# Performance work log

Hardware: AMD Instinct MI355X
Metric: run time of the kernel (lower is better)

## Reference

```python
import jax, jax.numpy as jnp
import numpy as np

GAMMA = 2.5
K = 4
RHO = 0.085
TAU_CLIP = 5.0
NUM_HEADS = 8


def setup_inputs() -> dict:
    key = jax.random.key(0)
    ks = jax.random.split(key, 4)
    B, T, C = 2, 2048, 512
    x = jax.random.normal(ks[0], (B, T, C), jnp.float32)
    tau = jax.random.uniform(ks[1], (B, T, T), jnp.float32)
    s = 1.0 / np.sqrt(C)
    Wqkv = jax.random.normal(ks[2], (C, 3 * C), jnp.float32) * s
    bqkv = jnp.zeros((3 * C,), jnp.float32)
    Wproj = jax.random.normal(ks[3], (C, C), jnp.float32) * s
    bproj = jnp.zeros((C,), jnp.float32)
    return dict(x=x, tau=tau, Wqkv=Wqkv, bqkv=bqkv, Wproj=Wproj, bproj=bproj)


def reference(x, tau, Wqkv, bqkv, Wproj, bproj):
    B, T, C = x.shape
    H = NUM_HEADS
    D = C // H
    qkv = x @ Wqkv + bqkv                       # [B,T,3C]
    q, k, v = jnp.split(qkv, 3, axis=-1)
    q = q.reshape(B, T, H, D).transpose(0, 2, 1, 3)   # [B,H,T,D]
    k = k.reshape(B, T, H, D).transpose(0, 2, 1, 3)
    v = v.reshape(B, T, H, D).transpose(0, 2, 1, 3)
    scale = D ** -0.5
    logits = jnp.einsum('bhtd,bhsd->bhts', q, k) * scale   # [B,H,T,T]
    pheromone_bias = GAMMA * jnp.log(tau + 1e-8)           # [B,T,T]
    logits = logits + pheromone_bias[:, None]
    # top-K keys per query from tau define the sparse mask (LOCAL_WINDOW=0)
    k_val = min(K, T)
    idx = jax.lax.top_k(tau, k_val)[1]                     # [B,T,K]
    mask = jnp.zeros((B, T, T), bool).at[
        jnp.arange(B)[:, None, None], jnp.arange(T)[None, :, None], idx
    ].set(True)
    logits = jnp.where(mask[:, None], logits, -jnp.inf)
    attn = jax.nn.softmax(logits, axis=-1)                 # [B,H,T,T]
    # EMA pheromone (tau) update, no gradient in original (torch.no_grad)
    signal = attn.mean(axis=1)                             # [B,T,T]
    tau_new = (1.0 - RHO) * tau + signal ** 3
    tau_new = tau_new / (tau_new.sum(axis=-1, keepdims=True) + 1e-8)
    tau_new = jnp.minimum(tau_new, TAU_CLIP)
    tau_new = jax.lax.stop_gradient(tau_new)
    out = jnp.einsum('bhts,bhsd->bthd', attn, v).reshape(B, T, C)
    out = out @ Wproj + bproj
    return out, tau_new
```

## Files before the change

kernel.cpp:

```cpp
#include <hip/hip_runtime.h>
#include <hip/hip_bf16.h>
#include <math.h>

#define BB 2
#define TT 2048
#define CC 512
#define HH 8
#define DD 64
#define KK 4
#define C3 1536
#define MROWS (BB*TT)

#define G1_NT (C3/64)
#define G1_BLOCKS (G1_NT*(MROWS/128))
#define G2_NT (CC/64)
#define G2_BLOCKS (G2_NT*(MROWS/128))

typedef __attribute__((ext_vector_type(8))) short bf16x8;
typedef __attribute__((ext_vector_type(4))) float floatx4;

static __device__ __forceinline__ unsigned short f2bf(float f) {
  unsigned int u = __float_as_uint(f);
  return (unsigned short)((u + 0x7fffu + ((u >> 16) & 1u)) >> 16);
}
static __device__ __forceinline__ float bf2f(unsigned short u) {
  return __uint_as_float(((unsigned int)u) << 16);
}

template<bool BF16OUT>
static __device__ __forceinline__ void gemm_body(
    int bid, int nt,
    const unsigned short* __restrict__ A,
    const unsigned short* __restrict__ Bt,
    const float* __restrict__ bias,
    void* __restrict__ Cout, int N, int K) {
  __shared__ bf16x8 As[128 * 4];
  __shared__ bf16x8 Bs[64 * 4];
  const int tid  = threadIdx.x;
  const int wave = tid >> 6;
  const int lane = tid & 63;
  const int n0 = (bid % nt) * 64;
  const int m0 = (bid / nt) * 128;
  const int m_off = (wave >> 1) * 64;
  const int n_off = (wave & 1) * 32;
  const int lrow = lane >> 2;
  const int lcol = (lane & 3) * 8;
  const int fr = lane & 15;
  const int fq = lane >> 4;

  floatx4 acc[4][2];
#pragma unroll
  for (int i = 0; i < 4; ++i)
#pragma unroll
    for (int j = 0; j < 2; ++j) acc[i][j] = (floatx4){0.f, 0.f, 0.f, 0.f};

  for (int k0 = 0; k0 < K; k0 += 32) {
#pragma unroll
    for (int s = 0; s < 2; ++s) {
      int q = wave * 2 + s;
      const unsigned short* ga = A + (size_t)(m0 + q * 16 + lrow) * K + k0 + lcol;
      __builtin_amdgcn_global_load_lds(
          (const __attribute__((address_space(1))) void*)ga,
          (__attribute__((address_space(3))) void*)((char*)As + q * 1024), 16, 0, 0);
    }
    const unsigned short* gb = Bt + (size_t)(n0 + wave * 16 + lrow) * K + k0 + lcol;
    __builtin_amdgcn_global_load_lds(
        (const __attribute__((address_space(1))) void*)gb,
        (__attribute__((address_space(3))) void*)((char*)Bs + wave * 1024), 16, 0, 0);
    __syncthreads();
    bf16x8 a[4], b[2];
#pragma unroll
    for (int i = 0; i < 4; ++i) a[i] = As[(m_off + i * 16 + fr) * 4 + fq];
#pragma unroll
    for (int j = 0; j < 2; ++j) b[j] = Bs[(n_off + j * 16 + fr) * 4 + fq];
#pragma unroll
    for (int i = 0; i < 4; ++i)
#pragma unroll
      for (int j = 0; j < 2; ++j)
        acc[i][j] = __builtin_amdgcn_mfma_f32_16x16x32_bf16(a[i], b[j], acc[i][j], 0, 0, 0);
    __syncthreads();
  }
#pragma unroll
  for (int j = 0; j < 2; ++j) {
    int col = n0 + n_off + j * 16 + fr;
    float bv = bias[col];
#pragma unroll
    for (int i = 0; i < 4; ++i) {
#pragma unroll
      for (int r = 0; r < 4; ++r) {
        int row = m0 + m_off + i * 16 + fq * 4 + r;
        float v = acc[i][j][r] + bv;
        if (BF16OUT) ((unsigned short*)Cout)[(size_t)row * N + col] = f2bf(v);
        else         ((float*)Cout)[(size_t)row * N + col] = v;
      }
    }
  }
}

static __device__ __forceinline__ void topk_body(
    int row, const float* __restrict__ tau, int* __restrict__ idx_out) {
  const int tid = threadIdx.x;
  const float4* rp = (const float4*)(tau + (size_t)row * TT);
  float v[8];
  float4 f0 = rp[tid * 2], f1 = rp[tid * 2 + 1];
  v[0]=f0.x; v[1]=f0.y; v[2]=f0.z; v[3]=f0.w;
  v[4]=f1.x; v[5]=f1.y; v[6]=f1.z; v[7]=f1.w;
  __shared__ float wv[4];
  __shared__ int wi[4];
  __shared__ int winner;
  const int base = tid * 8;
  int chosen[KK];
  for (int r = 0; r < KK; ++r) {
    float bv = v[0]; int bi = base;
#pragma unroll
    for (int i = 1; i < 8; ++i)
      if (v[i] > bv) { bv = v[i]; bi = base + i; }
#pragma unroll
    for (int off = 32; off > 0; off >>= 1) {
      float vv = __shfl_xor(bv, off, 64);
      int   ii = __shfl_xor(bi, off, 64);
      if (vv > bv || (vv == bv && ii < bi)) { bv = vv; bi = ii; }
    }
    if ((tid & 63) == 0) { wv[tid >> 6] = bv; wi[tid >> 6] = bi; }
    __syncthreads();
    if (tid == 0) {
      float b2 = wv[0]; int i2 = wi[0];
      for (int k = 1; k < 4; ++k)
        if (wv[k] > b2 || (wv[k] == b2 && wi[k] < i2)) { b2 = wv[k]; i2 = wi[k]; }
      winner = i2;
    }
    __syncthreads();
    int win = winner;
    chosen[r] = win;
    if ((win >> 3) == tid) v[win & 7] = -1e30f;
    __syncthreads();
  }
  if (tid < KK) idx_out[row * KK + tid] = chosen[tid];
}

static __device__ __forceinline__ void tau_body(
    int row, const float* __restrict__ tau, const int* __restrict__ idx_in,
    const float* __restrict__ sig_in, float* __restrict__ tau_out) {
  const int tid = threadIdx.x;
  int i4[KK]; float s3[KK];
#pragma unroll
  for (int j = 0; j < KK; ++j) {
    i4[j] = idx_in[row * KK + j];
    float s = sig_in[row * KK + j];
    s3[j] = s * s * s;
  }
  const float4* rp = (const float4*)(tau + (size_t)row * TT);
  float v[8];
  float4 f0 = rp[tid * 2], f1 = rp[tid * 2 + 1];
  v[0]=f0.x; v[1]=f0.y; v[2]=f0.z; v[3]=f0.w;
  v[4]=f1.x; v[5]=f1.y; v[6]=f1.z; v[7]=f1.w;
  const float keep = 1.0f - 0.085f;
  const int base = tid * 8;
  float local = 0.f;
#pragma unroll
  for (int i = 0; i < 8; ++i) {
    float t = keep * v[i];
#pragma unroll
    for (int j = 0; j < KK; ++j)
      if (base + i == i4[j]) t += s3[j];
    v[i] = t;
    local += t;
  }
#pragma unroll
  for (int off = 32; off > 0; off >>= 1) local += __shfl_xor(local, off, 64);
  __shared__ float wsum[4];
  __shared__ float tot;
  if ((tid & 63) == 0) wsum[tid >> 6] = local;
  __syncthreads();
  if (tid == 0) tot = wsum[0] + wsum[1] + wsum[2] + wsum[3];
  __syncthreads();
  float inv = 1.f / (tot + 1e-8f);
  float4* op = (float4*)(tau_out + (size_t)row * TT);
  float4 o0 = { fminf(v[0]*inv,5.f), fminf(v[1]*inv,5.f), fminf(v[2]*inv,5.f), fminf(v[3]*inv,5.f) };
  float4 o1 = { fminf(v[4]*inv,5.f), fminf(v[5]*inv,5.f), fminf(v[6]*inv,5.f), fminf(v[7]*inv,5.f) };
  op[tid * 2] = o0;
  op[tid * 2 + 1] = o1;
}

static __device__ __forceinline__ void transpose_body(
    int t, int nbx, const float* __restrict__ W, unsigned short* __restrict__ Wt,
    int R, int Cn) {
  __shared__ unsigned short tile[32][33];
  const int c0 = (t % nbx) * 32, r0 = (t / nbx) * 32;
  const int tx = threadIdx.x & 31, ty = threadIdx.x >> 5;
#pragma unroll
  for (int i = 0; i < 4; ++i) {
    int r = ty + i * 8;
    tile[r][tx] = f2bf(W[(size_t)(r0 + r) * Cn + c0 + tx]);
  }
  __syncthreads();
#pragma unroll
  for (int i = 0; i < 4; ++i) {
    int r = ty + i * 8;
    Wt[(size_t)(c0 + r) * R + r0 + tx] = tile[tx][r];
  }
}

__global__ __launch_bounds__(256) void prep_kernel(
    const float* __restrict__ x, unsigned short* __restrict__ x_bf,
    const float* __restrict__ Wqkv, unsigned short* __restrict__ wqkv_t,
    const float* __restrict__ Wproj, unsigned short* __restrict__ wproj_t) {
  const int bid = blockIdx.x;
  if (bid < 1024) {
    int g = bid * 256 + threadIdx.x;
    const float4* p = (const float4*)x;
    float4 f0 = p[g * 2], f1 = p[g * 2 + 1];
    union { unsigned short u[8]; uint4 v; } pk;
    pk.u[0]=f2bf(f0.x); pk.u[1]=f2bf(f0.y); pk.u[2]=f2bf(f0.z); pk.u[3]=f2bf(f0.w);
    pk.u[4]=f2bf(f1.x); pk.u[5]=f2bf(f1.y); pk.u[6]=f2bf(f1.z); pk.u[7]=f2bf(f1.w);
    ((uint4*)x_bf)[g] = pk.v;
  } else if (bid < 1024 + 768) {
    transpose_body(bid - 1024, C3 / 32, Wqkv, wqkv_t, CC, C3);
  } else {
    transpose_body(bid - 1792, CC / 32, Wproj, wproj_t, CC, CC);
  }
}

__global__ __launch_bounds__(256) void gemm1_topk_kernel(
    const unsigned short* __restrict__ x_bf,
    const unsigned short* __restrict__ wqkv_t,
    const float* __restrict__ bqkv, unsigned short* __restrict__ qkv_bf,
    const float* __restrict__ tau, int* __restrict__ idx_out) {
  if (blockIdx.x < G1_BLOCKS)
    gemm_body<true>(blockIdx.x, G1_NT, x_bf, wqkv_t, bqkv, qkv_bf, C3, CC);
  else
    topk_body(blockIdx.x - G1_BLOCKS, tau, idx_out);
}

__global__ __launch_bounds__(512) void attn_kernel(
    const unsigned short* __restrict__ qkv, const float* __restrict__ tau,
    const int* __restrict__ idx_in, unsigned short* __restrict__ attn_bf,
    float* __restrict__ sig_out) {
  const int row  = blockIdx.x;
  const int b    = row >> 11;
  const int tid  = threadIdx.x;
  const int h    = tid >> 6;
  const int lane = tid & 63;

  __shared__ int   idx4[KK];
  __shared__ float tau4[KK];
  __shared__ float ps[HH][KK];
  if (tid < KK) {
    int s = idx_in[row * KK + tid];
    idx4[tid] = s;
    tau4[tid] = tau[(size_t)row * TT + s];
  }
  __syncthreads();

  const float q = bf2f(qkv[(size_t)row * C3 + h * DD + lane]);
  int   sidx[KK];
  float logit[KK];
#pragma unroll
  for (int j = 0; j < KK; ++j) {
    sidx[j] = idx4[j];
    float kv = bf2f(qkv[((size_t)(b * TT + sidx[j])) * C3 + CC + h * DD + lane]);
    float p = q * kv;
#pragma unroll
    for (int off = 32; off > 0; off >>= 1) p += __shfl_xor(p, off, 64);
    logit[j] = p * 0.125f + 2.5f * logf(tau4[j] + 1e-8f);
  }

  float m = fmaxf(fmaxf(logit[0], logit[1]), fmaxf(logit[2], logit[3]));
  float p[KK], den = 0.f;
#pragma unroll
  for (int j = 0; j < KK; ++j) { p[j] = expf(logit[j] - m); den += p[j]; }
  float inv = 1.f / den;
#pragma unroll
  for (int j = 0; j < KK; ++j) p[j] *= inv;

  float o = 0.f;
#pragma unroll
  for (int j = 0; j < KK; ++j)
    o += p[j] * bf2f(qkv[((size_t)(b * TT + sidx[j])) * C3 + 2 * CC + h * DD + lane]);
  attn_bf[(size_t)row * CC + h * DD + lane] = f2bf(o);

  if (lane < KK) ps[h][lane] = p[lane];
  __syncthreads();
  if (tid < KK) {
    float s = 0.f;
#pragma unroll
    for (int k = 0; k < HH; ++k) s += ps[k][tid];
    sig_out[row * KK + tid] = s * (1.0f / HH);
  }
}

__global__ __launch_bounds__(256) void gemm2_tau_kernel(
    const unsigned short* __restrict__ attn_bf,
    const unsigned short* __restrict__ wproj_t,
    const float* __restrict__ bproj, float* __restrict__ out,
    const float* __restrict__ tau, const int* __restrict__ idx_in,
    const float* __restrict__ sig_in, float* __restrict__ tau_out) {
  if (blockIdx.x < G2_BLOCKS)
    gemm_body<false>(blockIdx.x, G2_NT, attn_bf, wproj_t, bproj, out, CC, CC);
  else
    tau_body(blockIdx.x - G2_BLOCKS, tau, idx_in, sig_in, tau_out);
}

extern "C" void kernel_launch(void* const* d_in, const int* in_sizes, int n_in,
                              void* d_out, int out_size, void* d_ws, size_t ws_size,
                              hipStream_t stream) {
  const float* x     = (const float*)d_in[0];
  const float* tau   = (const float*)d_in[1];
  const float* Wqkv  = (const float*)d_in[2];
  const float* bqkv  = (const float*)d_in[3];
  const float* Wproj = (const float*)d_in[4];
  const float* bproj = (const float*)d_in[5];

  float* out     = (float*)d_out;
  float* tau_new = out + (size_t)MROWS * CC;

  char* w = (char*)d_ws;
  unsigned short* qkv_bf  = (unsigned short*)w; w += (size_t)MROWS * C3 * 2;
  unsigned short* x_bf    = (unsigned short*)w; w += (size_t)MROWS * CC * 2;
  unsigned short* wqkv_t  = (unsigned short*)w; w += (size_t)C3 * CC * 2;
  unsigned short* wproj_t = (unsigned short*)w; w += (size_t)CC * CC * 2;
  unsigned short* attn_bf = (unsigned short*)w; w += (size_t)MROWS * CC * 2;
  int*   idx = (int*)w;                  w += (size_t)MROWS * KK * 4;
  float* sig = (float*)w;

  prep_kernel<<<2048, 256, 0, stream>>>(x, x_bf, Wqkv, wqkv_t, Wproj, wproj_t);

  gemm1_topk_kernel<<<G1_BLOCKS + MROWS, 256, 0, stream>>>(
      x_bf, wqkv_t, bqkv, qkv_bf, tau, idx);

  attn_kernel<<<MROWS, 512, 0, stream>>>(qkv_bf, tau, idx, attn_bf, sig);

  gemm2_tau_kernel<<<G2_BLOCKS + MROWS, 256, 0, stream>>>(
      attn_bf, wproj_t, bproj, out, tau, idx, sig, tau_new);
}
```

Baseline: 150.6 us.

## Widen GEMM tiles to 128x128, use nontemporal stores, batch attention gathers

The GEMM tiles grow from 128x64 to 128x128 per block, so each wave computes a 64x64 sub-tile with 16 MFMAs per k-step, which doubles A-tile reuse and halves the block count. Float outputs and the tau_out rows are written with nontemporal stores to avoid polluting the cache. In the sparse attention kernel, all K and V gathers are issued up front and the four dot-product reductions are interleaved, which exposes memory and shuffle parallelism. The cost is fewer blocks (less occupancy and tail balance) and more accumulator registers.

```diff
diff --git a/kernel.cpp b/kernel.cpp
--- a/kernel.cpp
+++ b/kernel.cpp
@@ -11,9 +11,9 @@
 #define C3 1536
 #define MROWS (BB*TT)
 
-#define G1_NT (C3/64)
+#define G1_NT (C3/128)
 #define G1_BLOCKS (G1_NT*(MROWS/128))
-#define G2_NT (CC/64)
+#define G2_NT (CC/128)
 #define G2_BLOCKS (G2_NT*(MROWS/128))
 
 typedef __attribute__((ext_vector_type(8))) short bf16x8;
@@ -35,24 +35,24 @@
     const float* __restrict__ bias,
     void* __restrict__ Cout, int N, int K) {
   __shared__ bf16x8 As[128 * 4];
-  __shared__ bf16x8 Bs[64 * 4];
+  __shared__ bf16x8 Bs[128 * 4];
   const int tid  = threadIdx.x;
   const int wave = tid >> 6;
   const int lane = tid & 63;
-  const int n0 = (bid % nt) * 64;
+  const int n0 = (bid % nt) * 128;
   const int m0 = (bid / nt) * 128;
   const int m_off = (wave >> 1) * 64;
-  const int n_off = (wave & 1) * 32;
+  const int n_off = (wave & 1) * 64;
   const int lrow = lane >> 2;
   const int lcol = (lane & 3) * 8;
   const int fr = lane & 15;
   const int fq = lane >> 4;
 
-  floatx4 acc[4][2];
+  floatx4 acc[4][4];
 #pragma unroll
   for (int i = 0; i < 4; ++i)
 #pragma unroll
-    for (int j = 0; j < 2; ++j) acc[i][j] = (floatx4){0.f, 0.f, 0.f, 0.f};
+    for (int j = 0; j < 4; ++j) acc[i][j] = (floatx4){0.f, 0.f, 0.f, 0.f};
 
   for (int k0 = 0; k0 < K; k0 += 32) {
 #pragma unroll
@@ -62,26 +62,26 @@
       __builtin_amdgcn_global_load_lds(
           (const __attribute__((address_space(1))) void*)ga,
           (__attribute__((address_space(3))) void*)((char*)As + q * 1024), 16, 0, 0);
+      const unsigned short* gb = Bt + (size_t)(n0 + q * 16 + lrow) * K + k0 + lcol;
+      __builtin_amdgcn_global_load_lds(
+          (const __attribute__((address_space(1))) void*)gb,
+          (__attribute__((address_space(3))) void*)((char*)Bs + q * 1024), 16, 0, 0);
     }
-    const unsigned short* gb = Bt + (size_t)(n0 + wave * 16 + lrow) * K + k0 + lcol;
-    __builtin_amdgcn_global_load_lds(
-        (const __attribute__((address_space(1))) void*)gb,
-        (__attribute__((address_space(3))) void*)((char*)Bs + wave * 1024), 16, 0, 0);
-    __syncthreads();
-    bf16x8 a[4], b[2];
+    __syncthreads();
+    bf16x8 a[4], b[4];
 #pragma unroll
     for (int i = 0; i < 4; ++i) a[i] = As[(m_off + i * 16 + fr) * 4 + fq];
 #pragma unroll
-    for (int j = 0; j < 2; ++j) b[j] = Bs[(n_off + j * 16 + fr) * 4 + fq];
+    for (int j = 0; j < 4; ++j) b[j] = Bs[(n_off + j * 16 + fr) * 4 + fq];
 #pragma unroll
     for (int i = 0; i < 4; ++i)
 #pragma unroll
-      for (int j = 0; j < 2; ++j)
+      for (int j = 0; j < 4; ++j)
         acc[i][j] = __builtin_amdgcn_mfma_f32_16x16x32_bf16(a[i], b[j], acc[i][j], 0, 0, 0);
     __syncthreads();
   }
 #pragma unroll
-  for (int j = 0; j < 2; ++j) {
+  for (int j = 0; j < 4; ++j) {
     int col = n0 + n_off + j * 16 + fr;
     float bv = bias[col];
 #pragma unroll
@@ -91,7 +91,10 @@
         int row = m0 + m_off + i * 16 + fq * 4 + r;
         float v = acc[i][j][r] + bv;
         if (BF16OUT) ((unsigned short*)Cout)[(size_t)row * N + col] = f2bf(v);
-        else         ((float*)Cout)[(size_t)row * N + col] = v;
+        else {
+          float* p = (float*)Cout + (size_t)row * N + col;
+          __builtin_nontemporal_store(v, p);
+        }
       }
     }
   }
@@ -175,11 +178,11 @@
   if (tid == 0) tot = wsum[0] + wsum[1] + wsum[2] + wsum[3];
   __syncthreads();
   float inv = 1.f / (tot + 1e-8f);
-  float4* op = (float4*)(tau_out + (size_t)row * TT);
-  float4 o0 = { fminf(v[0]*inv,5.f), fminf(v[1]*inv,5.f), fminf(v[2]*inv,5.f), fminf(v[3]*inv,5.f) };
-  float4 o1 = { fminf(v[4]*inv,5.f), fminf(v[5]*inv,5.f), fminf(v[6]*inv,5.f), fminf(v[7]*inv,5.f) };
-  op[tid * 2] = o0;
-  op[tid * 2 + 1] = o1;
+  floatx4* op = (floatx4*)(tau_out + (size_t)row * TT);
+  floatx4 o0 = { fminf(v[0]*inv,5.f), fminf(v[1]*inv,5.f), fminf(v[2]*inv,5.f), fminf(v[3]*inv,5.f) };
+  floatx4 o1 = { fminf(v[4]*inv,5.f), fminf(v[5]*inv,5.f), fminf(v[6]*inv,5.f), fminf(v[7]*inv,5.f) };
+  __builtin_nontemporal_store(o0, op + tid * 2);
+  __builtin_nontemporal_store(o1, op + tid * 2 + 1);
 }
 
 static __device__ __forceinline__ void transpose_body(
@@ -253,20 +256,29 @@
   __syncthreads();
 
   const float q = bf2f(qkv[(size_t)row * C3 + h * DD + lane]);
-  int   sidx[KK];
+  float kv[KK], vv[KK];
+#pragma unroll
+  for (int j = 0; j < KK; ++j) {
+    size_t bs = ((size_t)(b * TT + idx4[j])) * C3 + h * DD + lane;
+    kv[j] = bf2f(qkv[bs + CC]);
+    vv[j] = bf2f(qkv[bs + 2 * CC]);
+  }
+
+  float p[KK];
+#pragma unroll
+  for (int j = 0; j < KK; ++j) p[j] = q * kv[j];
+#pragma unroll
+  for (int off = 32; off > 0; off >>= 1)
+#pragma unroll
+    for (int j = 0; j < KK; ++j) p[j] += __shfl_xor(p[j], off, 64);
+
   float logit[KK];
 #pragma unroll
-  for (int j = 0; j < KK; ++j) {
-    sidx[j] = idx4[j];
-    float kv = bf2f(qkv[((size_t)(b * TT + sidx[j])) * C3 + CC + h * DD + lane]);
-    float p = q * kv;
-#pragma unroll
-    for (int off = 32; off > 0; off >>= 1) p += __shfl_xor(p, off, 64);
-    logit[j] = p * 0.125f + 2.5f * logf(tau4[j] + 1e-8f);
-  }
+  for (int j = 0; j < KK; ++j)
+    logit[j] = p[j] * 0.125f + 2.5f * logf(tau4[j] + 1e-8f);
 
   float m = fmaxf(fmaxf(logit[0], logit[1]), fmaxf(logit[2], logit[3]));
-  float p[KK], den = 0.f;
+  float den = 0.f;
 #pragma unroll
   for (int j = 0; j < KK; ++j) { p[j] = expf(logit[j] - m); den += p[j]; }
   float inv = 1.f / den;
@@ -275,8 +287,7 @@
 
   float o = 0.f;
 #pragma unroll
-  for (int j = 0; j < KK; ++j)
-    o += p[j] * bf2f(qkv[((size_t)(b * TT + sidx[j])) * C3 + 2 * CC + h * DD + lane]);
+  for (int j = 0; j < KK; ++j) o += p[j] * vv[j];
   attn_bf[(size_t)row * CC + h * DD + lane] = f2bf(o);
 
   if (lane < KK) ps[h][lane] = p[lane];
```

Measured after the change: 163.0 us. 1.08x slower.

## Fuse top-k, attention and tau update into one kernel; swizzle GEMM LDS

Applied to the files above, without the earlier changes.

Top-k selection, sparse attention and the EMA tau update now run in one per-row kernel, so each tau row is read once instead of three times and the idx/sig buffers are gone. The GEMM kernels lose their co-scheduled side work and become plain launches. The GEMM LDS tile layout gets an XOR swizzle meant to cut bank conflicts on fragment reads. In exchange, top-k now runs serially before attention, no longer overlapped with GEMM1, and the fused kernel carries more barriers per row.

```diff
diff --git a/kernel.cpp b/kernel.cpp
--- a/kernel.cpp
+++ b/kernel.cpp
@@ -10,11 +10,6 @@
 #define KK 4
 #define C3 1536
 #define MROWS (BB*TT)
-
-#define G1_NT (C3/64)
-#define G1_BLOCKS (G1_NT*(MROWS/128))
-#define G2_NT (CC/64)
-#define G2_BLOCKS (G2_NT*(MROWS/128))
 
 typedef __attribute__((ext_vector_type(8))) short bf16x8;
 typedef __attribute__((ext_vector_type(4))) float floatx4;
@@ -44,9 +39,10 @@
   const int m_off = (wave >> 1) * 64;
   const int n_off = (wave & 1) * 32;
   const int lrow = lane >> 2;
-  const int lcol = (lane & 3) * 8;
+  const int lx   = ((lane & 3) ^ ((lane >> 3) & 3)) * 8;
   const int fr = lane & 15;
   const int fq = lane >> 4;
+  const int key = (fr >> 1) & 3;
 
   floatx4 acc[4][2];
 #pragma unroll
@@ -58,21 +54,23 @@
 #pragma unroll
     for (int s = 0; s < 2; ++s) {
       int q = wave * 2 + s;
-      const unsigned short* ga = A + (size_t)(m0 + q * 16 + lrow) * K + k0 + lcol;
+      const unsigned short* ga = A + (size_t)(m0 + q * 16 + lrow) * K + k0 + lx;
       __builtin_amdgcn_global_load_lds(
           (const __attribute__((address_space(1))) void*)ga,
           (__attribute__((address_space(3))) void*)((char*)As + q * 1024), 16, 0, 0);
     }
-    const unsigned short* gb = Bt + (size_t)(n0 + wave * 16 + lrow) * K + k0 + lcol;
+    const unsigned short* gb = Bt + (size_t)(n0 + wave * 16 + lrow) * K + k0 + lx;
     __builtin_amdgcn_global_load_lds(
         (const __attribute__((address_space(1))) void*)gb,
         (__attribute__((address_space(3))) void*)((char*)Bs + wave * 1024), 16, 0, 0);
     __syncthreads();
     bf16x8 a[4], b[2];
 #pragma unroll
-    for (int i = 0; i < 4; ++i) a[i] = As[(m_off + i * 16 + fr) * 4 + fq];
-#pragma unroll
-    for (int j = 0; j < 2; ++j) b[j] = Bs[(n_off + j * 16 + fr) * 4 + fq];
+    for (int i = 0; i < 4; ++i)
+      a[i] = As[(m_off + i * 16 + fr) * 4 + (fq ^ key)];
+#pragma unroll
+    for (int j = 0; j < 2; ++j)
+      b[j] = Bs[(n_off + j * 16 + fr) * 4 + (fq ^ key)];
 #pragma unroll
     for (int i = 0; i < 4; ++i)
 #pragma unroll
@@ -95,91 +93,6 @@
       }
     }
   }
-}
-
-static __device__ __forceinline__ void topk_body(
-    int row, const float* __restrict__ tau, int* __restrict__ idx_out) {
-  const int tid = threadIdx.x;
-  const float4* rp = (const float4*)(tau + (size_t)row * TT);
-  float v[8];
-  float4 f0 = rp[tid * 2], f1 = rp[tid * 2 + 1];
-  v[0]=f0.x; v[1]=f0.y; v[2]=f0.z; v[3]=f0.w;
-  v[4]=f1.x; v[5]=f1.y; v[6]=f1.z; v[7]=f1.w;
-  __shared__ float wv[4];
-  __shared__ int wi[4];
-  __shared__ int winner;
-  const int base = tid * 8;
-  int chosen[KK];
-  for (int r = 0; r < KK; ++r) {
-    float bv = v[0]; int bi = base;
-#pragma unroll
-    for (int i = 1; i < 8; ++i)
-      if (v[i] > bv) { bv = v[i]; bi = base + i; }
-#pragma unroll
-    for (int off = 32; off > 0; off >>= 1) {
-      float vv = __shfl_xor(bv, off, 64);
-      int   ii = __shfl_xor(bi, off, 64);
-      if (vv > bv || (vv == bv && ii < bi)) { bv = vv; bi = ii; }
-    }
-    if ((tid & 63) == 0) { wv[tid >> 6] = bv; wi[tid >> 6] = bi; }
-    __syncthreads();
-    if (tid == 0) {
-      float b2 = wv[0]; int i2 = wi[0];
-      for (int k = 1; k < 4; ++k)
-        if (wv[k] > b2 || (wv[k] == b2 && wi[k] < i2)) { b2 = wv[k]; i2 = wi[k]; }
-      winner = i2;
-    }
-    __syncthreads();
-    int win = winner;
-    chosen[r] = win;
-    if ((win >> 3) == tid) v[win & 7] = -1e30f;
-    __syncthreads();
-  }
-  if (tid < KK) idx_out[row * KK + tid] = chosen[tid];
-}
-
-static __device__ __forceinline__ void tau_body(
-    int row, const float* __restrict__ tau, const int* __restrict__ idx_in,
-    const float* __restrict__ sig_in, float* __restrict__ tau_out) {
-  const int tid = threadIdx.x;
-  int i4[KK]; float s3[KK];
-#pragma unroll
-  for (int j = 0; j < KK; ++j) {
-    i4[j] = idx_in[row * KK + j];
-    float s = sig_in[row * KK + j];
-    s3[j] = s * s * s;
-  }
-  const float4* rp = (const float4*)(tau + (size_t)row * TT);
-  float v[8];
-  float4 f0 = rp[tid * 2], f1 = rp[tid * 2 + 1];
-  v[0]=f0.x; v[1]=f0.y; v[2]=f0.z; v[3]=f0.w;
-  v[4]=f1.x; v[5]=f1.y; v[6]=f1.z; v[7]=f1.w;
-  const float keep = 1.0f - 0.085f;
-  const int base = tid * 8;
-  float local = 0.f;
-#pragma unroll
-  for (int i = 0; i < 8; ++i) {
-    float t = keep * v[i];
-#pragma unroll
-    for (int j = 0; j < KK; ++j)
-      if (base + i == i4[j]) t += s3[j];
-    v[i] = t;
-    local += t;
-  }
-#pragma unroll
-  for (int off = 32; off > 0; off >>= 1) local += __shfl_xor(local, off, 64);
-  __shared__ float wsum[4];
-  __shared__ float tot;
-  if ((tid & 63) == 0) wsum[tid >> 6] = local;
-  __syncthreads();
-  if (tid == 0) tot = wsum[0] + wsum[1] + wsum[2] + wsum[3];
-  __syncthreads();
-  float inv = 1.f / (tot + 1e-8f);
-  float4* op = (float4*)(tau_out + (size_t)row * TT);
-  float4 o0 = { fminf(v[0]*inv,5.f), fminf(v[1]*inv,5.f), fminf(v[2]*inv,5.f), fminf(v[3]*inv,5.f) };
-  float4 o1 = { fminf(v[4]*inv,5.f), fminf(v[5]*inv,5.f), fminf(v[6]*inv,5.f), fminf(v[7]*inv,5.f) };
-  op[tid * 2] = o0;
-  op[tid * 2 + 1] = o1;
 }
 
 static __device__ __forceinline__ void transpose_body(
@@ -221,52 +134,81 @@
   }
 }
 
-__global__ __launch_bounds__(256) void gemm1_topk_kernel(
+__global__ __launch_bounds__(256) void gemm1_kernel(
     const unsigned short* __restrict__ x_bf,
     const unsigned short* __restrict__ wqkv_t,
-    const float* __restrict__ bqkv, unsigned short* __restrict__ qkv_bf,
-    const float* __restrict__ tau, int* __restrict__ idx_out) {
-  if (blockIdx.x < G1_BLOCKS)
-    gemm_body<true>(blockIdx.x, G1_NT, x_bf, wqkv_t, bqkv, qkv_bf, C3, CC);
-  else
-    topk_body(blockIdx.x - G1_BLOCKS, tau, idx_out);
-}
-
-__global__ __launch_bounds__(512) void attn_kernel(
-    const unsigned short* __restrict__ qkv, const float* __restrict__ tau,
-    const int* __restrict__ idx_in, unsigned short* __restrict__ attn_bf,
-    float* __restrict__ sig_out) {
+    const float* __restrict__ bqkv,
+    unsigned short* __restrict__ qkv_bf) {
+  gemm_body<true>(blockIdx.x, C3 / 64, x_bf, wqkv_t, bqkv, qkv_bf, C3, CC);
+}
+
+__global__ __launch_bounds__(512) void fused_attn_kernel(
+    const unsigned short* __restrict__ qkv,
+    const float* __restrict__ tau,
+    unsigned short* __restrict__ attn_bf,
+    float* __restrict__ tau_new) {
   const int row  = blockIdx.x;
   const int b    = row >> 11;
   const int tid  = threadIdx.x;
-  const int h    = tid >> 6;
+  const int wave = tid >> 6;
   const int lane = tid & 63;
-
+  const int h    = wave;
+
+  float4 f = ((const float4*)(tau + (size_t)row * TT))[tid];
+  float v[4] = { f.x, f.y, f.z, f.w };
+  const int base = tid * 4;
+
+  __shared__ float wv8[8];
+  __shared__ int   wi8[8];
   __shared__ int   idx4[KK];
   __shared__ float tau4[KK];
-  __shared__ float ps[HH][KK];
-  if (tid < KK) {
-    int s = idx_in[row * KK + tid];
-    idx4[tid] = s;
-    tau4[tid] = tau[(size_t)row * TT + s];
-  }
-  __syncthreads();
+  for (int r = 0; r < KK; ++r) {
+    float bv = v[0]; int bi = base;
+#pragma unroll
+    for (int i = 1; i < 4; ++i)
+      if (v[i] > bv) { bv = v[i]; bi = base + i; }
+#pragma unroll
+    for (int off = 32; off > 0; off >>= 1) {
+      float vv = __shfl_xor(bv, off, 64);
+      int   ii = __shfl_xor(bi, off, 64);
+      if (vv > bv || (vv == bv && ii < bi)) { bv = vv; bi = ii; }
+    }
+    if (lane == 0) { wv8[wave] = bv; wi8[wave] = bi; }
+    __syncthreads();
+    if (tid == 0) {
+      float b2 = wv8[0]; int i2 = wi8[0];
+#pragma unroll
+      for (int k = 1; k < 8; ++k)
+        if (wv8[k] > b2 || (wv8[k] == b2 && wi8[k] < i2)) { b2 = wv8[k]; i2 = wi8[k]; }
+      idx4[r] = i2; tau4[r] = b2;
+    }
+    __syncthreads();
+    int win = idx4[r];
+    if ((win >> 2) == tid) v[win & 3] = -1e30f;
+  }
 
   const float q = bf2f(qkv[(size_t)row * C3 + h * DD + lane]);
-  int   sidx[KK];
+  float kj[KK], vj[KK];
+#pragma unroll
+  for (int j = 0; j < KK; ++j) {
+    size_t bs = ((size_t)(b * TT + idx4[j])) * C3 + h * DD + lane;
+    kj[j] = bf2f(qkv[bs + CC]);
+    vj[j] = bf2f(qkv[bs + 2 * CC]);
+  }
+  float p[KK];
+#pragma unroll
+  for (int j = 0; j < KK; ++j) p[j] = q * kj[j];
+#pragma unroll
+  for (int off = 32; off > 0; off >>= 1)
+#pragma unroll
+    for (int j = 0; j < KK; ++j) p[j] += __shfl_xor(p[j], off, 64);
+
   float logit[KK];
 #pragma unroll
-  for (int j = 0; j < KK; ++j) {
-    sidx[j] = idx4[j];
-    float kv = bf2f(qkv[((size_t)(b * TT + sidx[j])) * C3 + CC + h * DD + lane]);
-    float p = q * kv;
-#pragma unroll
-    for (int off = 32; off > 0; off >>= 1) p += __shfl_xor(p, off, 64);
-    logit[j] = p * 0.125f + 2.5f * logf(tau4[j] + 1e-8f);
-  }
-
+  for (int j = 0; j < KK; ++j)
+    logit[j] = p[j] * 0.125f + 2.5f * logf(tau4[j] + 1e-8f);
   float m = fmaxf(fmaxf(logit[0], logit[1]), fmaxf(logit[2], logit[3]));
-  float p[KK], den = 0.f;
+  float den = 0.f;
 #pragma unroll
   for (int j = 0; j < KK; ++j) { p[j] = expf(logit[j] - m); den += p[j]; }
   float inv = 1.f / den;
@@ -275,30 +217,59 @@
 
   float o = 0.f;
 #pragma unroll
-  for (int j = 0; j < KK; ++j)
-    o += p[j] * bf2f(qkv[((size_t)(b * TT + sidx[j])) * C3 + 2 * CC + h * DD + lane]);
+  for (int j = 0; j < KK; ++j) o += p[j] * vj[j];
   attn_bf[(size_t)row * CC + h * DD + lane] = f2bf(o);
 
+  __shared__ float ps[HH][KK];
+  __shared__ float s3sh[KK];
   if (lane < KK) ps[h][lane] = p[lane];
   __syncthreads();
   if (tid < KK) {
     float s = 0.f;
 #pragma unroll
     for (int k = 0; k < HH; ++k) s += ps[k][tid];
-    sig_out[row * KK + tid] = s * (1.0f / HH);
-  }
-}
-
-__global__ __launch_bounds__(256) void gemm2_tau_kernel(
+    s *= (1.0f / HH);
+    s3sh[tid] = s * s * s;
+  }
+  __syncthreads();
+
+  const float keep = 1.0f - 0.085f;
+  float t4[4];
+  float local = 0.f;
+#pragma unroll
+  for (int i = 0; i < 4; ++i) {
+    float t = keep * v[i];
+#pragma unroll
+    for (int j = 0; j < KK; ++j)
+      if (base + i == idx4[j]) t = keep * tau4[j] + s3sh[j];
+    t4[i] = t;
+    local += t;
+  }
+#pragma unroll
+  for (int off = 32; off > 0; off >>= 1) local += __shfl_xor(local, off, 64);
+  __shared__ float wsum[8];
+  __shared__ float tot;
+  if (lane == 0) wsum[wave] = local;
+  __syncthreads();
+  if (tid == 0) {
+    float s = 0.f;
+#pragma unroll
+    for (int k = 0; k < 8; ++k) s += wsum[k];
+    tot = s;
+  }
+  __syncthreads();
+  float ninv = 1.f / (tot + 1e-8f);
+  float4 o4 = { fminf(t4[0] * ninv, 5.f), fminf(t4[1] * ninv, 5.f),
+                fminf(t4[2] * ninv, 5.f), fminf(t4[3] * ninv, 5.f) };
+  ((float4*)(tau_new + (size_t)row * TT))[tid] = o4;
+}
+
+__global__ __launch_bounds__(256) void gemm2_kernel(
     const unsigned short* __restrict__ attn_bf,
     const unsigned short* __restrict__ wproj_t,
-    const float* __restrict__ bproj, float* __restrict__ out,
-    const float* __restrict__ tau, const int* __restrict__ idx_in,
-    const float* __restrict__ sig_in, float* __restrict__ tau_out) {
-  if (blockIdx.x < G2_BLOCKS)
-    gemm_body<false>(blockIdx.x, G2_NT, attn_bf, wproj_t, bproj, out, CC, CC);
-  else
-    tau_body(blockIdx.x - G2_BLOCKS, tau, idx_in, sig_in, tau_out);
+    const float* __restrict__ bproj,
+    float* __restrict__ out) {
+  gemm_body<false>(blockIdx.x, CC / 64, attn_bf, wproj_t, bproj, out, CC, CC);
 }
 
 extern "C" void kernel_launch(void* const* d_in, const int* in_sizes, int n_in,
@@ -319,17 +290,15 @@
   unsigned short* x_bf    = (unsigned short*)w; w += (size_t)MROWS * CC * 2;
   unsigned short* wqkv_t  = (unsigned short*)w; w += (size_t)C3 * CC * 2;
   unsigned short* wproj_t = (unsigned short*)w; w += (size_t)CC * CC * 2;
-  unsigned short* attn_bf = (unsigned short*)w; w += (size_t)MROWS * CC * 2;
-  int*   idx = (int*)w;                  w += (size_t)MROWS * KK * 4;
-  float* sig = (float*)w;
+  unsigned short* attn_bf = (unsigned short*)w;
 
   prep_kernel<<<2048, 256, 0, stream>>>(x, x_bf, Wqkv, wqkv_t, Wproj, wproj_t);
 
-  gemm1_topk_kernel<<<G1_BLOCKS + MROWS, 256, 0, stream>>>(
-      x_bf, wqkv_t, bqkv, qkv_bf, tau, idx);
-
-  attn_kernel<<<MROWS, 512, 0, stream>>>(qkv_bf, tau, idx, attn_bf, sig);
-
-  gemm2_tau_kernel<<<G2_BLOCKS + MROWS, 256, 0, stream>>>(
-      attn_bf, wproj_t, bproj, out, tau, idx, sig, tau_new);
-}
+  gemm1_kernel<<<(MROWS / 128) * (C3 / 64), 256, 0, stream>>>(
+      x_bf, wqkv_t, bqkv, qkv_bf);
+
+  fused_attn_kernel<<<MROWS, 512, 0, stream>>>(qkv_bf, tau, attn_bf, tau_new);
+
+  gemm2_kernel<<<(MROWS / 128) * (CC / 64), 256, 0, stream>>>(
+      attn_bf, wproj_t, bproj, out);
+}
```

Result: slower. 166.5 us (+10.6%).
